# Optimization experiments

Measured on AMD Instinct MI355X. Metric: run time of the kernel, lower is better.

The kernel has to match this reference:

```python
import jax, jax.numpy as jnp
import numpy as np

N_NODES = 50000
N_EDGES = 1_600_000
IN_DIM = 64
HID_DIM = 64
OUT_DIM = 64


def setup_inputs() -> dict:
    key = jax.random.key(0)
    k = jax.random.split(key, 7)
    feat = jax.random.normal(k[0], (N_NODES, IN_DIM), dtype=jnp.float32)
    src = jax.random.randint(k[1], (N_EDGES,), 0, N_NODES, dtype=jnp.int32)
    dst = jax.random.randint(k[2], (N_EDGES,), 0, N_NODES, dtype=jnp.int32)
    # nn.init.normal_(weight, std=0.1); bias default uniform ~ small, use 0.1*randn
    W1 = 0.1 * jax.random.normal(k[3], (HID_DIM, IN_DIM), dtype=jnp.float32)
    b1 = 0.1 * jax.random.normal(k[4], (HID_DIM,), dtype=jnp.float32)
    W2 = 0.1 * jax.random.normal(k[5], (OUT_DIM, HID_DIM), dtype=jnp.float32)
    b2 = 0.1 * jax.random.normal(k[6], (OUT_DIM,), dtype=jnp.float32)
    return {"feat": feat, "src": src, "dst": dst, "W1": W1, "b1": b1, "W2": W2, "b2": b2}


def _gnn_layer(h, src, dst, W, b):
    # copy_u + sum: gather source-node features along edges, scatter-sum to dst
    agg = jax.ops.segment_sum(h[src], dst, num_segments=N_NODES)  # [N, d_in]
    return agg @ W.T + b  # nn.Linear


def reference(feat, src, dst, W1, b1, W2, b2):
    h = _gnn_layer(feat, src, dst, W1, b1)
    h = jnp.tanh(h)
    h = _gnn_layer(h, src, dst, W2, b2)
    return h
```

## Files before the change

kernel.cpp:

```cpp
#include <hip/hip_runtime.h>

#define N_NODES 50000
#define N_EDGES 1600000
#define DIM 64
#define NBK 196
#define BIN_BLOCKS 391
#define CSR_CAP 12288
#define QCAP 3072
#define GEMM_BLOCKS 197

__device__ __forceinline__ unsigned short f2bf(float f) {
    union { float f; unsigned u; } v; v.f = f;
    unsigned r = v.u + 0x7FFF + ((v.u >> 16) & 1);
    return (unsigned short)(r >> 16);
}
__device__ __forceinline__ float bf_lo(unsigned u) {
    union { unsigned u; float f; } v; v.u = u << 16;  return v.f;
}
__device__ __forceinline__ float bf_hi(unsigned u) {
    union { unsigned u; float f; } v; v.u = u & 0xFFFF0000u;  return v.f;
}
__device__ __forceinline__ float bf2f(unsigned short h) {
    union { unsigned u; float f; } v; v.u = ((unsigned)h) << 16;  return v.f;
}

__global__ __launch_bounds__(256) void bin_and_gemm1(const int* __restrict__ src,
                                                     const int* __restrict__ dst,
                                                     int* __restrict__ bcur,
                                                     int* __restrict__ binned,
                                                     const float* __restrict__ X,
                                                     const float* __restrict__ W,
                                                     unsigned short* __restrict__ T) {
    __shared__ int cnt[NBK];
    __shared__ int lofs[NBK];
    __shared__ int shiftv[NBK];
    __shared__ int sb[256];
    __shared__ int stag[4096];
    __shared__ unsigned char stb[4096];
    __shared__ float Ws[64 * 64];
    int tid = threadIdx.x;

    if (blockIdx.x >= BIN_BLOCKS) {
#pragma unroll
        for (int j = 0; j < 16; ++j) Ws[j * 256 + tid] = W[j * 256 + tid];
        __syncthreads();

        int n = (blockIdx.x - BIN_BLOCKS) * 256 + tid;
        if (n > N_NODES) return;
        ushort4* tp = (ushort4*)(T + (size_t)n * 64);
        if (n == N_NODES) {
            ushort4 z = {0, 0, 0, 0};
#pragma unroll
            for (int k = 0; k < 16; ++k) tp[k] = z;
            return;
        }

        float4 x[16];
        const float4* xp = (const float4*)(X + (size_t)n * 64);
#pragma unroll
        for (int k = 0; k < 16; ++k) x[k] = xp[k];

        for (int fg = 0; fg < 16; ++fg) {
            float r[4];
#pragma unroll
            for (int fi = 0; fi < 4; ++fi) {
                int f = fg * 4 + fi;
                float acc = 0.f;
#pragma unroll
                for (int k4 = 0; k4 < 16; ++k4) {
                    float4 w = *(const float4*)&Ws[f * 64 + k4 * 4];
                    float4 xv = x[k4];
                    acc += xv.x * w.x + xv.y * w.y + xv.z * w.z + xv.w * w.w;
                }
                r[fi] = acc;
            }
            ushort4 o;
            o.x = f2bf(r[0]); o.y = f2bf(r[1]); o.z = f2bf(r[2]); o.w = f2bf(r[3]);
            tp[fg] = o;
        }
        return;
    }

    if (tid < NBK) cnt[tid] = 0;
    __syncthreads();

    int base = blockIdx.x * 4096;
    int nedge = N_EDGES - base;
    if (nedge > 4096) nedge = 4096;

    int myb[16], myr[16], myp[16];
#pragma unroll
    for (int i = 0; i < 16; ++i) {
        int e = base + i * 256 + tid;
        myb[i] = -1;
        if (e < N_EDGES) {
            int s = src[e], d = dst[e];
            int b = d >> 8;
            myb[i] = b;
            myp[i] = ((d & 255) << 16) | s;
            myr[i] = atomicAdd(&cnt[b], 1);
        }
    }
    __syncthreads();

    int c = (tid < NBK) ? cnt[tid] : 0;
    sb[tid] = c;
    __syncthreads();
    for (int off = 1; off < 256; off <<= 1) {
        int u = (tid >= off) ? sb[tid - off] : 0;
        __syncthreads();
        sb[tid] += u;
        __syncthreads();
    }
    if (tid < NBK) {
        lofs[tid] = sb[tid] - c;
        if (c) shiftv[tid] = tid * CSR_CAP + atomicAdd(&bcur[tid * 16], c) - lofs[tid];
    }
    __syncthreads();

#pragma unroll
    for (int i = 0; i < 16; ++i) {
        if (myb[i] >= 0) {
            int idx = lofs[myb[i]] + myr[i];
            stag[idx] = myp[i];
            stb[idx] = (unsigned char)myb[i];
        }
    }
    __syncthreads();

    for (int i = tid; i < nedge; i += 256)
        binned[i + shiftv[stb[i]]] = stag[i];
}

__global__ __launch_bounds__(256) void build_csr(const int* __restrict__ binned,
                                                 const int* __restrict__ bcur,
                                                 unsigned* __restrict__ nodeinfo,
                                                 unsigned short* __restrict__ csr16) {
    __shared__ int cnt[64], cnt2[64], ofs[64], sb[64];
    __shared__ int qtot;
    int tid = threadIdx.x;
    int b = blockIdx.x >> 2;
    int q = blockIdx.x & 3;
    int ibase = b * CSR_CAP;
    int qbase = (b * 4 + q) * QCAP;
    int m = bcur[b * 16];
    if (m > CSR_CAP) m = CSR_CAP;
    if (tid < 64) { cnt[tid] = 0; cnt2[tid] = 0; }
    __syncthreads();

    for (int i = tid; i < m; i += 256) {
        int dl = (binned[ibase + i] >> 16) & 255;
        if ((dl >> 6) == q) atomicAdd(&cnt[dl & 63], 1);
    }
    __syncthreads();

    int v = 0;
    if (tid < 64) { v = (cnt[tid] + 15) & ~15; sb[tid] = v; }
    __syncthreads();
    for (int off = 1; off < 64; off <<= 1) {
        int u = (tid >= off && tid < 64) ? sb[tid - off] : 0;
        __syncthreads();
        if (tid < 64) sb[tid] += u;
        __syncthreads();
    }
    if (tid < 64) {
        ofs[tid] = sb[tid] - v;
        int node = (b << 8) + (q << 6) + tid;
        if (node < N_NODES)
            nodeinfo[node] = ((unsigned)v << 23) | (unsigned)(qbase + ofs[tid]);
    }
    if (tid == 63) qtot = sb[63];
    __syncthreads();

    int qt = qtot;
    for (int i = tid; i < qt; i += 256) csr16[qbase + i] = (unsigned short)N_NODES;
    __syncthreads();

    for (int i = tid; i < m; i += 256) {
        int p = binned[ibase + i];
        int dl = (p >> 16) & 255;
        if ((dl >> 6) == q) {
            int r = atomicAdd(&cnt2[dl & 63], 1);
            csr16[qbase + ofs[dl & 63] + r] = (unsigned short)(p & 0xFFFF);
        }
    }
}

__global__ __launch_bounds__(256) void gemm64_bf16(const unsigned short* __restrict__ X,
                                                   const float* __restrict__ W,
                                                   unsigned short* __restrict__ T,
                                                   int n_rows) {
    __shared__ float Ws[64 * 64];
    int tid = threadIdx.x;
#pragma unroll
    for (int j = 0; j < 16; ++j) Ws[j * 256 + tid] = W[j * 256 + tid];
    __syncthreads();

    int n = blockIdx.x * 256 + tid;
    if (n >= n_rows) {
        if (n == n_rows) {
            ushort4 z = {0, 0, 0, 0};
            ushort4* tp = (ushort4*)(T + (size_t)n * 64);
#pragma unroll
            for (int k = 0; k < 16; ++k) tp[k] = z;
        }
        return;
    }

    uint4 xr[8];
    const uint4* xp = (const uint4*)(X + (size_t)n * 64);
#pragma unroll
    for (int k = 0; k < 8; ++k) xr[k] = xp[k];
    float x[64];
    const unsigned* xu = (const unsigned*)xr;
#pragma unroll
    for (int p = 0; p < 32; ++p) {
        unsigned u = xu[p];
        x[2 * p] = bf_lo(u);
        x[2 * p + 1] = bf_hi(u);
    }

    const float4* xv4 = (const float4*)x;
    ushort4* tp = (ushort4*)(T + (size_t)n * 64);
    for (int fg = 0; fg < 16; ++fg) {
        float r[4];
#pragma unroll
        for (int fi = 0; fi < 4; ++fi) {
            int f = fg * 4 + fi;
            float acc = 0.f;
#pragma unroll
            for (int k4 = 0; k4 < 16; ++k4) {
                float4 w = *(const float4*)&Ws[f * 64 + k4 * 4];
                float4 xv = xv4[k4];
                acc += xv.x * w.x + xv.y * w.y + xv.z * w.z + xv.w * w.w;
            }
            r[fi] = acc;
        }
        ushort4 o;
        o.x = f2bf(r[0]); o.y = f2bf(r[1]); o.z = f2bf(r[2]); o.w = f2bf(r[3]);
        tp[fg] = o;
    }
}

__global__ __launch_bounds__(256) void aggregate(const unsigned short* __restrict__ T,
                                                 const unsigned short* __restrict__ csr,
                                                 const unsigned* __restrict__ nodeinfo,
                                                 const float* __restrict__ bias,
                                                 void* __restrict__ outp,
                                                 int mode) {
    int node = blockIdx.x * 4 + (threadIdx.x >> 6);
    int lane = threadIdx.x & 63;
    if (node >= N_NODES) return;
    unsigned info = nodeinfo[node];
    int pos = (int)(info & 0x7FFFFFu);
    int groups = (int)(info >> 23) >> 3;
    const uint4* ix = (const uint4*)(csr + pos);
    float acc = bias[lane];
    float acc2 = 0.f;
    for (int g = 0; g < groups; g += 2) {
        uint4 ia = ix[g];
        uint4 ib = ix[g + 1];
        int s0 = ia.x & 0xFFFF, s1 = ia.x >> 16;
        int s2 = ia.y & 0xFFFF, s3 = ia.y >> 16;
        int s4 = ia.z & 0xFFFF, s5 = ia.z >> 16;
        int s6 = ia.w & 0xFFFF, s7 = ia.w >> 16;
        int u0 = ib.x & 0xFFFF, u1 = ib.x >> 16;
        int u2 = ib.y & 0xFFFF, u3 = ib.y >> 16;
        int u4 = ib.z & 0xFFFF, u5 = ib.z >> 16;
        int u6 = ib.w & 0xFFFF, u7 = ib.w >> 16;
        unsigned short v0 = T[(size_t)s0 * DIM + lane];
        unsigned short v1 = T[(size_t)s1 * DIM + lane];
        unsigned short v2 = T[(size_t)s2 * DIM + lane];
        unsigned short v3 = T[(size_t)s3 * DIM + lane];
        unsigned short v4 = T[(size_t)s4 * DIM + lane];
        unsigned short v5 = T[(size_t)s5 * DIM + lane];
        unsigned short v6 = T[(size_t)s6 * DIM + lane];
        unsigned short v7 = T[(size_t)s7 * DIM + lane];
        unsigned short w0 = T[(size_t)u0 * DIM + lane];
        unsigned short w1 = T[(size_t)u1 * DIM + lane];
        unsigned short w2 = T[(size_t)u2 * DIM + lane];
        unsigned short w3 = T[(size_t)u3 * DIM + lane];
        unsigned short w4 = T[(size_t)u4 * DIM + lane];
        unsigned short w5 = T[(size_t)u5 * DIM + lane];
        unsigned short w6 = T[(size_t)u6 * DIM + lane];
        unsigned short w7 = T[(size_t)u7 * DIM + lane];
        acc  += (bf2f(v0) + bf2f(v1)) + (bf2f(v2) + bf2f(v3)) +
                (bf2f(v4) + bf2f(v5)) + (bf2f(v6) + bf2f(v7));
        acc2 += (bf2f(w0) + bf2f(w1)) + (bf2f(w2) + bf2f(w3)) +
                (bf2f(w4) + bf2f(w5)) + (bf2f(w6) + bf2f(w7));
    }
    acc += acc2;
    if (mode) {
        float e = __expf(2.f * acc);
        acc = 1.f - 2.f / (e + 1.f);
        ((unsigned short*)outp)[(size_t)node * DIM + lane] = f2bf(acc);
    } else {
        ((float*)outp)[(size_t)node * DIM + lane] = acc;
    }
}

extern "C" void kernel_launch(void* const* d_in, const int* in_sizes, int n_in,
                              void* d_out, int out_size, void* d_ws, size_t ws_size,
                              hipStream_t stream) {
    const float* feat = (const float*)d_in[0];
    const int*   src  = (const int*)d_in[1];
    const int*   dst  = (const int*)d_in[2];
    const float* W1   = (const float*)d_in[3];
    const float* b1   = (const float*)d_in[4];
    const float* W2   = (const float*)d_in[5];
    const float* b2   = (const float*)d_in[6];

    int*            binned   = (int*)d_ws;
    unsigned short* csr16    = (unsigned short*)(binned + NBK * CSR_CAP);
    unsigned*       nodeinfo = (unsigned*)(csr16 + NBK * 4 * QCAP);
    int*            bcur     = (int*)(nodeinfo + N_NODES);
    unsigned short* t        = (unsigned short*)(bcur + NBK * 16 + 8);

    unsigned short* h = (unsigned short*)d_out;
    float* out = (float*)d_out;

    const int NB = (N_NODES + 3) / 4;

    hipMemsetAsync(bcur, 0, NBK * 16 * sizeof(int), stream);
    bin_and_gemm1<<<BIN_BLOCKS + GEMM_BLOCKS, 256, 0, stream>>>(
        src, dst, bcur, binned, feat, W1, t);
    build_csr<<<NBK * 4, 256, 0, stream>>>(binned, bcur, nodeinfo, csr16);

    aggregate<<<NB, 256, 0, stream>>>(t, csr16, nodeinfo, b1, h, 1);

    gemm64_bf16<<<GEMM_BLOCKS, 256, 0, stream>>>(h, W2, t, N_NODES);
    aggregate<<<NB, 256, 0, stream>>>(t, csr16, nodeinfo, b2, out, 0);
}
```

Measured before the change: 243.9 us.

## Split feature table into two half-planes and gather 16-byte rows per lane in aggregate

The transformed feature table is stored as two 32-column bf16 planes instead of one 64-column array. The aggregate kernel launches twice as many blocks, one per half. Each wavefront handles 16 edges per iteration, with each lane loading 16 bytes (8 features) of one neighbour row, followed by a cross-lane shuffle reduction. This swaps many 2-byte scalar gathers for fewer wide vector loads, and each half-plane is a smaller working set that should fit better in cache. The cost is extra shuffle reduction work, index-selection logic, and twice as many index reads across blocks.

```diff
diff --git a/kernel.cpp b/kernel.cpp
--- a/kernel.cpp
+++ b/kernel.cpp
@@ -8,6 +8,8 @@
 #define CSR_CAP 12288
 #define QCAP 3072
 #define GEMM_BLOCKS 197
+#define NB_AGG 12500
+#define PLANE ((size_t)(N_NODES + 1) * 32)
 
 __device__ __forceinline__ unsigned short f2bf(float f) {
     union { float f; unsigned u; } v; v.f = f;
@@ -19,9 +21,6 @@
 }
 __device__ __forceinline__ float bf_hi(unsigned u) {
     union { unsigned u; float f; } v; v.u = u & 0xFFFF0000u;  return v.f;
-}
-__device__ __forceinline__ float bf2f(unsigned short h) {
-    union { unsigned u; float f; } v; v.u = ((unsigned)h) << 16;  return v.f;
 }
 
 __global__ __launch_bounds__(256) void bin_and_gemm1(const int* __restrict__ src,
@@ -30,7 +29,8 @@
                                                      int* __restrict__ binned,
                                                      const float* __restrict__ X,
                                                      const float* __restrict__ W,
-                                                     unsigned short* __restrict__ T) {
+                                                     unsigned short* __restrict__ T0,
+                                                     unsigned short* __restrict__ T1) {
     __shared__ int cnt[NBK];
     __shared__ int lofs[NBK];
     __shared__ int shiftv[NBK];
@@ -47,11 +47,12 @@
 
         int n = (blockIdx.x - BIN_BLOCKS) * 256 + tid;
         if (n > N_NODES) return;
-        ushort4* tp = (ushort4*)(T + (size_t)n * 64);
+        ushort4* t0 = (ushort4*)(T0 + (size_t)n * 32);
+        ushort4* t1 = (ushort4*)(T1 + (size_t)n * 32);
         if (n == N_NODES) {
             ushort4 z = {0, 0, 0, 0};
 #pragma unroll
-            for (int k = 0; k < 16; ++k) tp[k] = z;
+            for (int k = 0; k < 8; ++k) { t0[k] = z; t1[k] = z; }
             return;
         }
 
@@ -76,7 +77,7 @@
             }
             ushort4 o;
             o.x = f2bf(r[0]); o.y = f2bf(r[1]); o.z = f2bf(r[2]); o.w = f2bf(r[3]);
-            tp[fg] = o;
+            if (fg < 8) t0[fg] = o; else t1[fg - 8] = o;
         }
         return;
     }
@@ -188,7 +189,8 @@
 
 __global__ __launch_bounds__(256) void gemm64_bf16(const unsigned short* __restrict__ X,
                                                    const float* __restrict__ W,
-                                                   unsigned short* __restrict__ T,
+                                                   unsigned short* __restrict__ T0,
+                                                   unsigned short* __restrict__ T1,
                                                    int n_rows) {
     __shared__ float Ws[64 * 64];
     int tid = threadIdx.x;
@@ -197,13 +199,13 @@
     __syncthreads();
 
     int n = blockIdx.x * 256 + tid;
-    if (n >= n_rows) {
-        if (n == n_rows) {
-            ushort4 z = {0, 0, 0, 0};
-            ushort4* tp = (ushort4*)(T + (size_t)n * 64);
-#pragma unroll
-            for (int k = 0; k < 16; ++k) tp[k] = z;
-        }
+    if (n > n_rows) return;
+    ushort4* t0 = (ushort4*)(T0 + (size_t)n * 32);
+    ushort4* t1 = (ushort4*)(T1 + (size_t)n * 32);
+    if (n == n_rows) {
+        ushort4 z = {0, 0, 0, 0};
+#pragma unroll
+        for (int k = 0; k < 8; ++k) { t0[k] = z; t1[k] = z; }
         return;
     }
 
@@ -221,7 +223,6 @@
     }
 
     const float4* xv4 = (const float4*)x;
-    ushort4* tp = (ushort4*)(T + (size_t)n * 64);
     for (int fg = 0; fg < 16; ++fg) {
         float r[4];
 #pragma unroll
@@ -238,64 +239,77 @@
         }
         ushort4 o;
         o.x = f2bf(r[0]); o.y = f2bf(r[1]); o.z = f2bf(r[2]); o.w = f2bf(r[3]);
-        tp[fg] = o;
-    }
-}
-
-__global__ __launch_bounds__(256) void aggregate(const unsigned short* __restrict__ T,
+        if (fg < 8) t0[fg] = o; else t1[fg - 8] = o;
+    }
+}
+
+__global__ __launch_bounds__(256) void aggregate(const unsigned short* __restrict__ T0,
+                                                 const unsigned short* __restrict__ T1,
                                                  const unsigned short* __restrict__ csr,
                                                  const unsigned* __restrict__ nodeinfo,
                                                  const float* __restrict__ bias,
                                                  void* __restrict__ outp,
                                                  int mode) {
-    int node = blockIdx.x * 4 + (threadIdx.x >> 6);
+    int bidx = blockIdx.x;
+    int half = 0;
+    if (bidx >= NB_AGG) { half = 1; bidx -= NB_AGG; }
+    int node = bidx * 4 + (threadIdx.x >> 6);
     int lane = threadIdx.x & 63;
-    if (node >= N_NODES) return;
     unsigned info = nodeinfo[node];
     int pos = (int)(info & 0x7FFFFFu);
-    int groups = (int)(info >> 23) >> 3;
+    int iters = (int)(info >> 23) >> 4;
+    int j = lane >> 2;
+    int s4 = lane & 3;
+    int c = (j >> 1) & 3;
     const uint4* ix = (const uint4*)(csr + pos);
-    float acc = bias[lane];
-    float acc2 = 0.f;
-    for (int g = 0; g < groups; g += 2) {
-        uint4 ia = ix[g];
-        uint4 ib = ix[g + 1];
-        int s0 = ia.x & 0xFFFF, s1 = ia.x >> 16;
-        int s2 = ia.y & 0xFFFF, s3 = ia.y >> 16;
-        int s4 = ia.z & 0xFFFF, s5 = ia.z >> 16;
-        int s6 = ia.w & 0xFFFF, s7 = ia.w >> 16;
-        int u0 = ib.x & 0xFFFF, u1 = ib.x >> 16;
-        int u2 = ib.y & 0xFFFF, u3 = ib.y >> 16;
-        int u4 = ib.z & 0xFFFF, u5 = ib.z >> 16;
-        int u6 = ib.w & 0xFFFF, u7 = ib.w >> 16;
-        unsigned short v0 = T[(size_t)s0 * DIM + lane];
-        unsigned short v1 = T[(size_t)s1 * DIM + lane];
-        unsigned short v2 = T[(size_t)s2 * DIM + lane];
-        unsigned short v3 = T[(size_t)s3 * DIM + lane];
-        unsigned short v4 = T[(size_t)s4 * DIM + lane];
-        unsigned short v5 = T[(size_t)s5 * DIM + lane];
-        unsigned short v6 = T[(size_t)s6 * DIM + lane];
-        unsigned short v7 = T[(size_t)s7 * DIM + lane];
-        unsigned short w0 = T[(size_t)u0 * DIM + lane];
-        unsigned short w1 = T[(size_t)u1 * DIM + lane];
-        unsigned short w2 = T[(size_t)u2 * DIM + lane];
-        unsigned short w3 = T[(size_t)u3 * DIM + lane];
-        unsigned short w4 = T[(size_t)u4 * DIM + lane];
-        unsigned short w5 = T[(size_t)u5 * DIM + lane];
-        unsigned short w6 = T[(size_t)u6 * DIM + lane];
-        unsigned short w7 = T[(size_t)u7 * DIM + lane];
-        acc  += (bf2f(v0) + bf2f(v1)) + (bf2f(v2) + bf2f(v3)) +
-                (bf2f(v4) + bf2f(v5)) + (bf2f(v6) + bf2f(v7));
-        acc2 += (bf2f(w0) + bf2f(w1)) + (bf2f(w2) + bf2f(w3)) +
-                (bf2f(w4) + bf2f(w5)) + (bf2f(w6) + bf2f(w7));
-    }
-    acc += acc2;
-    if (mode) {
-        float e = __expf(2.f * acc);
-        acc = 1.f - 2.f / (e + 1.f);
-        ((unsigned short*)outp)[(size_t)node * DIM + lane] = f2bf(acc);
-    } else {
-        ((float*)outp)[(size_t)node * DIM + lane] = acc;
+    const char* Tb = (const char*)(half ? T1 : T0);
+    int fb = s4 * 16;
+
+    float a0 = 0.f, a1 = 0.f, a2 = 0.f, a3 = 0.f,
+          a4 = 0.f, a5 = 0.f, a6 = 0.f, a7 = 0.f;
+    for (int g = 0; g < iters; ++g) {
+        uint4 ia = ix[2 * g];
+        uint4 ib = ix[2 * g + 1];
+        uint4 sel = (j & 8) ? ib : ia;
+        unsigned w = (c == 0) ? sel.x : (c == 1) ? sel.y : (c == 2) ? sel.z : sel.w;
+        unsigned s = (j & 1) ? (w >> 16) : (w & 0xFFFFu);
+        uint4 r = *(const uint4*)(Tb + (size_t)s * 64 + fb);
+        a0 += bf_lo(r.x); a1 += bf_hi(r.x);
+        a2 += bf_lo(r.y); a3 += bf_hi(r.y);
+        a4 += bf_lo(r.z); a5 += bf_hi(r.z);
+        a6 += bf_lo(r.w); a7 += bf_hi(r.w);
+    }
+#pragma unroll
+    for (int mask = 4; mask <= 32; mask <<= 1) {
+        a0 += __shfl_xor(a0, mask, 64);
+        a1 += __shfl_xor(a1, mask, 64);
+        a2 += __shfl_xor(a2, mask, 64);
+        a3 += __shfl_xor(a3, mask, 64);
+        a4 += __shfl_xor(a4, mask, 64);
+        a5 += __shfl_xor(a5, mask, 64);
+        a6 += __shfl_xor(a6, mask, 64);
+        a7 += __shfl_xor(a7, mask, 64);
+    }
+    if (lane < 4) {
+        int col0 = half * 32 + lane * 8;
+        float av[8] = {a0, a1, a2, a3, a4, a5, a6, a7};
+#pragma unroll
+        for (int k = 0; k < 8; ++k) av[k] += bias[col0 + k];
+        if (mode) {
+            unsigned short hb[8];
+#pragma unroll
+            for (int k = 0; k < 8; ++k) {
+                float e = __expf(2.f * av[k]);
+                hb[k] = f2bf(1.f - 2.f / (e + 1.f));
+            }
+            ushort4* hp = (ushort4*)&((unsigned short*)outp)[(size_t)node * DIM + col0];
+            hp[0] = make_ushort4(hb[0], hb[1], hb[2], hb[3]);
+            hp[1] = make_ushort4(hb[4], hb[5], hb[6], hb[7]);
+        } else {
+            float4* op = (float4*)&((float*)outp)[(size_t)node * DIM + col0];
+            op[0] = make_float4(av[0], av[1], av[2], av[3]);
+            op[1] = make_float4(av[4], av[5], av[6], av[7]);
+        }
     }
 }
 
@@ -314,20 +328,19 @@
     unsigned short* csr16    = (unsigned short*)(binned + NBK * CSR_CAP);
     unsigned*       nodeinfo = (unsigned*)(csr16 + NBK * 4 * QCAP);
     int*            bcur     = (int*)(nodeinfo + N_NODES);
-    unsigned short* t        = (unsigned short*)(bcur + NBK * 16 + 8);
+    unsigned short* T0       = (unsigned short*)(bcur + NBK * 16 + 8);
+    unsigned short* T1       = T0 + PLANE;
 
     unsigned short* h = (unsigned short*)d_out;
     float* out = (float*)d_out;
 
-    const int NB = (N_NODES + 3) / 4;
-
     hipMemsetAsync(bcur, 0, NBK * 16 * sizeof(int), stream);
     bin_and_gemm1<<<BIN_BLOCKS + GEMM_BLOCKS, 256, 0, stream>>>(
-        src, dst, bcur, binned, feat, W1, t);
+        src, dst, bcur, binned, feat, W1, T0, T1);
     build_csr<<<NBK * 4, 256, 0, stream>>>(binned, bcur, nodeinfo, csr16);
 
-    aggregate<<<NB, 256, 0, stream>>>(t, csr16, nodeinfo, b1, h, 1);
-
-    gemm64_bf16<<<GEMM_BLOCKS, 256, 0, stream>>>(h, W2, t, N_NODES);
-    aggregate<<<NB, 256, 0, stream>>>(t, csr16, nodeinfo, b2, out, 0);
-}
+    aggregate<<<2 * NB_AGG, 256, 0, stream>>>(T0, T1, csr16, nodeinfo, b1, h, 1);
+
+    gemm64_bf16<<<GEMM_BLOCKS, 256, 0, stream>>>(h, W2, T0, T1, N_NODES);
+    aggregate<<<2 * NB_AGG, 256, 0, stream>>>(T0, T1, csr16, nodeinfo, b2, out, 0);
+}
```

New measurement: 313.7 us. +28.6%, slower.

## Count per-node degrees in binning pass and shrink shared memory and registers

Applied to the files above, without the earlier changes.

The binning kernel now keeps per-destination degree counts with global atomics, so build_csr no longer rescans the binned edges to count them. Padding fill becomes per-node. The two branches of the fused binning/GEMM kernel now share one union shared-memory buffer under a launch-bounds occupancy hint. Both GEMMs keep inputs packed as bf16 to cut register use, which also rounds layer-1 features to bf16 before the matmul. The cost is 1.6M extra global atomics on a 50k-entry array, plus a larger memset.

```diff
diff --git a/kernel.cpp b/kernel.cpp
--- a/kernel.cpp
+++ b/kernel.cpp
@@ -8,6 +8,7 @@
 #define CSR_CAP 12288
 #define QCAP 3072
 #define GEMM_BLOCKS 197
+#define NB_AGG 12500
 
 __device__ __forceinline__ unsigned short f2bf(float f) {
     union { float f; unsigned u; } v; v.f = f;
@@ -24,23 +25,19 @@
     union { unsigned u; float f; } v; v.u = ((unsigned)h) << 16;  return v.f;
 }
 
-__global__ __launch_bounds__(256) void bin_and_gemm1(const int* __restrict__ src,
-                                                     const int* __restrict__ dst,
-                                                     int* __restrict__ bcur,
-                                                     int* __restrict__ binned,
-                                                     const float* __restrict__ X,
-                                                     const float* __restrict__ W,
-                                                     unsigned short* __restrict__ T) {
-    __shared__ int cnt[NBK];
-    __shared__ int lofs[NBK];
-    __shared__ int shiftv[NBK];
-    __shared__ int sb[256];
-    __shared__ int stag[4096];
-    __shared__ unsigned char stb[4096];
-    __shared__ float Ws[64 * 64];
+__global__ __launch_bounds__(256, 4) void bin_and_gemm1(const int* __restrict__ src,
+                                                        const int* __restrict__ dst,
+                                                        int* __restrict__ bcur,
+                                                        int* __restrict__ ncnt,
+                                                        int* __restrict__ binned,
+                                                        const float* __restrict__ X,
+                                                        const float* __restrict__ W,
+                                                        unsigned short* __restrict__ T) {
+    __shared__ __align__(16) char smem[27008];
     int tid = threadIdx.x;
 
     if (blockIdx.x >= BIN_BLOCKS) {
+        float* Ws = (float*)smem;
 #pragma unroll
         for (int j = 0; j < 16; ++j) Ws[j * 256 + tid] = W[j * 256 + tid];
         __syncthreads();
@@ -55,10 +52,14 @@
             return;
         }
 
-        float4 x[16];
+        unsigned xq[32];
         const float4* xp = (const float4*)(X + (size_t)n * 64);
 #pragma unroll
-        for (int k = 0; k < 16; ++k) x[k] = xp[k];
+        for (int k = 0; k < 16; ++k) {
+            float4 xv = xp[k];
+            xq[2 * k]     = ((unsigned)f2bf(xv.y) << 16) | f2bf(xv.x);
+            xq[2 * k + 1] = ((unsigned)f2bf(xv.w) << 16) | f2bf(xv.z);
+        }
 
         for (int fg = 0; fg < 16; ++fg) {
             float r[4];
@@ -69,8 +70,9 @@
 #pragma unroll
                 for (int k4 = 0; k4 < 16; ++k4) {
                     float4 w = *(const float4*)&Ws[f * 64 + k4 * 4];
-                    float4 xv = x[k4];
-                    acc += xv.x * w.x + xv.y * w.y + xv.z * w.z + xv.w * w.w;
+                    unsigned p0 = xq[2 * k4], p1 = xq[2 * k4 + 1];
+                    acc += bf_lo(p0) * w.x + bf_hi(p0) * w.y +
+                           bf_lo(p1) * w.z + bf_hi(p1) * w.w;
                 }
                 r[fi] = acc;
             }
@@ -80,6 +82,13 @@
         }
         return;
     }
+
+    int* cnt    = (int*)smem;
+    int* lofs   = cnt + NBK;
+    int* shiftv = lofs + NBK;
+    int* sb     = shiftv + NBK;
+    int* stag   = sb + 256;
+    unsigned char* stb = (unsigned char*)(stag + 4096);
 
     if (tid < NBK) cnt[tid] = 0;
     __syncthreads();
@@ -99,6 +108,7 @@
             myb[i] = b;
             myp[i] = ((d & 255) << 16) | s;
             myr[i] = atomicAdd(&cnt[b], 1);
+            atomicAdd(&ncnt[d], 1);
         }
     }
     __syncthreads();
@@ -134,10 +144,10 @@
 
 __global__ __launch_bounds__(256) void build_csr(const int* __restrict__ binned,
                                                  const int* __restrict__ bcur,
+                                                 const int* __restrict__ ncnt,
                                                  unsigned* __restrict__ nodeinfo,
                                                  unsigned short* __restrict__ csr16) {
     __shared__ int cnt[64], cnt2[64], ofs[64], sb[64];
-    __shared__ int qtot;
     int tid = threadIdx.x;
     int b = blockIdx.x >> 2;
     int q = blockIdx.x & 3;
@@ -145,17 +155,16 @@
     int qbase = (b * 4 + q) * QCAP;
     int m = bcur[b * 16];
     if (m > CSR_CAP) m = CSR_CAP;
-    if (tid < 64) { cnt[tid] = 0; cnt2[tid] = 0; }
-    __syncthreads();
-
-    for (int i = tid; i < m; i += 256) {
-        int dl = (binned[ibase + i] >> 16) & 255;
-        if ((dl >> 6) == q) atomicAdd(&cnt[dl & 63], 1);
-    }
-    __syncthreads();
-
-    int v = 0;
-    if (tid < 64) { v = (cnt[tid] + 15) & ~15; sb[tid] = v; }
+    int node = (b << 8) + (q << 6) + tid;
+
+    int v = 0, c0 = 0;
+    if (tid < 64) {
+        c0 = (node < N_NODES) ? ncnt[node] : 0;
+        cnt[tid] = c0;
+        cnt2[tid] = 0;
+        v = (c0 + 15) & ~15;
+        sb[tid] = v;
+    }
     __syncthreads();
     for (int off = 1; off < 64; off <<= 1) {
         int u = (tid >= off && tid < 64) ? sb[tid - off] : 0;
@@ -165,15 +174,11 @@
     }
     if (tid < 64) {
         ofs[tid] = sb[tid] - v;
-        int node = (b << 8) + (q << 6) + tid;
         if (node < N_NODES)
             nodeinfo[node] = ((unsigned)v << 23) | (unsigned)(qbase + ofs[tid]);
-    }
-    if (tid == 63) qtot = sb[63];
-    __syncthreads();
-
-    int qt = qtot;
-    for (int i = tid; i < qt; i += 256) csr16[qbase + i] = (unsigned short)N_NODES;
+        int o = qbase + ofs[tid];
+        for (int i = c0; i < v; ++i) csr16[o + i] = (unsigned short)N_NODES;
+    }
     __syncthreads();
 
     for (int i = tid; i < m; i += 256) {
@@ -211,16 +216,8 @@
     const uint4* xp = (const uint4*)(X + (size_t)n * 64);
 #pragma unroll
     for (int k = 0; k < 8; ++k) xr[k] = xp[k];
-    float x[64];
-    const unsigned* xu = (const unsigned*)xr;
-#pragma unroll
-    for (int p = 0; p < 32; ++p) {
-        unsigned u = xu[p];
-        x[2 * p] = bf_lo(u);
-        x[2 * p + 1] = bf_hi(u);
-    }
-
-    const float4* xv4 = (const float4*)x;
+    const unsigned* xq = (const unsigned*)xr;
+
     ushort4* tp = (ushort4*)(T + (size_t)n * 64);
     for (int fg = 0; fg < 16; ++fg) {
         float r[4];
@@ -231,8 +228,9 @@
 #pragma unroll
             for (int k4 = 0; k4 < 16; ++k4) {
                 float4 w = *(const float4*)&Ws[f * 64 + k4 * 4];
-                float4 xv = xv4[k4];
-                acc += xv.x * w.x + xv.y * w.y + xv.z * w.z + xv.w * w.w;
+                unsigned p0 = xq[2 * k4], p1 = xq[2 * k4 + 1];
+                acc += bf_lo(p0) * w.x + bf_hi(p0) * w.y +
+                       bf_lo(p1) * w.z + bf_hi(p1) * w.w;
             }
             r[fi] = acc;
         }
@@ -314,20 +312,19 @@
     unsigned short* csr16    = (unsigned short*)(binned + NBK * CSR_CAP);
     unsigned*       nodeinfo = (unsigned*)(csr16 + NBK * 4 * QCAP);
     int*            bcur     = (int*)(nodeinfo + N_NODES);
-    unsigned short* t        = (unsigned short*)(bcur + NBK * 16 + 8);
+    int*            ncnt     = bcur + NBK * 16;
+    unsigned short* t        = (unsigned short*)(ncnt + N_NODES);
 
     unsigned short* h = (unsigned short*)d_out;
     float* out = (float*)d_out;
 
-    const int NB = (N_NODES + 3) / 4;
-
-    hipMemsetAsync(bcur, 0, NBK * 16 * sizeof(int), stream);
+    hipMemsetAsync(bcur, 0, (NBK * 16 + N_NODES) * sizeof(int), stream);
     bin_and_gemm1<<<BIN_BLOCKS + GEMM_BLOCKS, 256, 0, stream>>>(
-        src, dst, bcur, binned, feat, W1, t);
-    build_csr<<<NBK * 4, 256, 0, stream>>>(binned, bcur, nodeinfo, csr16);
-
-    aggregate<<<NB, 256, 0, stream>>>(t, csr16, nodeinfo, b1, h, 1);
+        src, dst, bcur, ncnt, binned, feat, W1, t);
+    build_csr<<<NBK * 4, 256, 0, stream>>>(binned, bcur, ncnt, nodeinfo, csr16);
+
+    aggregate<<<NB_AGG, 256, 0, stream>>>(t, csr16, nodeinfo, b1, h, 1);
 
     gemm64_bf16<<<GEMM_BLOCKS, 256, 0, stream>>>(h, W2, t, N_NODES);
-    aggregate<<<NB, 256, 0, stream>>>(t, csr16, nodeinfo, b2, out, 0);
-}
+    aggregate<<<NB_AGG, 256, 0, stream>>>(t, csr16, nodeinfo, b2, out, 0);
+}
```

After: 537.8 us. +120.5%, slower.

## Fuse layer-2 linear transform into first aggregation epilogue

Applied to the files above, without the earlier changes.

Removes the separate gemm64_bf16 kernel and the bf16 intermediate h buffer by having the first aggregation compute tanh into shared memory and immediately multiply by W2 (loaded transposed into LDS per block). Output goes to a separate workspace buffer t2, and the zero sentinel row is written by block 0. This saves one launch and one full round trip of node features through global memory, but each block now stages 16KB of W2 into LDS, which may reduce occupancy of the latency-bound gather kernel.

```diff
diff --git a/kernel.cpp b/kernel.cpp
--- a/kernel.cpp
+++ b/kernel.cpp
@@ -8,17 +8,12 @@
 #define CSR_CAP 12288
 #define QCAP 3072
 #define GEMM_BLOCKS 197
+#define NB_AGG 12500
 
 __device__ __forceinline__ unsigned short f2bf(float f) {
     union { float f; unsigned u; } v; v.f = f;
     unsigned r = v.u + 0x7FFF + ((v.u >> 16) & 1);
     return (unsigned short)(r >> 16);
-}
-__device__ __forceinline__ float bf_lo(unsigned u) {
-    union { unsigned u; float f; } v; v.u = u << 16;  return v.f;
-}
-__device__ __forceinline__ float bf_hi(unsigned u) {
-    union { unsigned u; float f; } v; v.u = u & 0xFFFF0000u;  return v.f;
 }
 __device__ __forceinline__ float bf2f(unsigned short h) {
     union { unsigned u; float f; } v; v.u = ((unsigned)h) << 16;  return v.f;
@@ -186,68 +181,87 @@
     }
 }
 
-__global__ __launch_bounds__(256) void gemm64_bf16(const unsigned short* __restrict__ X,
-                                                   const float* __restrict__ W,
-                                                   unsigned short* __restrict__ T,
-                                                   int n_rows) {
-    __shared__ float Ws[64 * 64];
-    int tid = threadIdx.x;
-#pragma unroll
-    for (int j = 0; j < 16; ++j) Ws[j * 256 + tid] = W[j * 256 + tid];
-    __syncthreads();
-
-    int n = blockIdx.x * 256 + tid;
-    if (n >= n_rows) {
-        if (n == n_rows) {
-            ushort4 z = {0, 0, 0, 0};
-            ushort4* tp = (ushort4*)(T + (size_t)n * 64);
-#pragma unroll
-            for (int k = 0; k < 16; ++k) tp[k] = z;
-        }
-        return;
-    }
-
-    uint4 xr[8];
-    const uint4* xp = (const uint4*)(X + (size_t)n * 64);
-#pragma unroll
-    for (int k = 0; k < 8; ++k) xr[k] = xp[k];
-    float x[64];
-    const unsigned* xu = (const unsigned*)xr;
-#pragma unroll
-    for (int p = 0; p < 32; ++p) {
-        unsigned u = xu[p];
-        x[2 * p] = bf_lo(u);
-        x[2 * p + 1] = bf_hi(u);
-    }
-
-    const float4* xv4 = (const float4*)x;
-    ushort4* tp = (ushort4*)(T + (size_t)n * 64);
-    for (int fg = 0; fg < 16; ++fg) {
-        float r[4];
-#pragma unroll
-        for (int fi = 0; fi < 4; ++fi) {
-            int f = fg * 4 + fi;
-            float acc = 0.f;
-#pragma unroll
-            for (int k4 = 0; k4 < 16; ++k4) {
-                float4 w = *(const float4*)&Ws[f * 64 + k4 * 4];
-                float4 xv = xv4[k4];
-                acc += xv.x * w.x + xv.y * w.y + xv.z * w.z + xv.w * w.w;
-            }
-            r[fi] = acc;
-        }
-        ushort4 o;
-        o.x = f2bf(r[0]); o.y = f2bf(r[1]); o.z = f2bf(r[2]); o.w = f2bf(r[3]);
-        tp[fg] = o;
-    }
-}
-
-__global__ __launch_bounds__(256) void aggregate(const unsigned short* __restrict__ T,
+__global__ __launch_bounds__(256) void agg_fuse1(const unsigned short* __restrict__ T,
                                                  const unsigned short* __restrict__ csr,
                                                  const unsigned* __restrict__ nodeinfo,
-                                                 const float* __restrict__ bias,
-                                                 void* __restrict__ outp,
-                                                 int mode) {
+                                                 const float* __restrict__ b1,
+                                                 const float* __restrict__ W2,
+                                                 unsigned short* __restrict__ T2) {
+    __shared__ float4 W2t4[1024];
+    __shared__ float hsf[4 * 64];
+    int tid = threadIdx.x;
+    int w = tid >> 6;
+    int lane = tid & 63;
+    int node = blockIdx.x * 4 + w;
+
+    for (int L4 = tid; L4 < 1024; L4 += 256) {
+        int k4 = L4 >> 6, f = L4 & 63;
+        W2t4[L4] = *(const float4*)(W2 + f * 64 + k4 * 4);
+    }
+
+    unsigned info = nodeinfo[node];
+    int pos = (int)(info & 0x7FFFFFu);
+    int groups = (int)(info >> 23) >> 3;
+    const uint4* ix = (const uint4*)(csr + pos);
+    float acc = b1[lane];
+    float acc2 = 0.f;
+    for (int g = 0; g < groups; g += 2) {
+        uint4 ia = ix[g];
+        uint4 ib = ix[g + 1];
+        int s0 = ia.x & 0xFFFF, s1 = ia.x >> 16;
+        int s2 = ia.y & 0xFFFF, s3 = ia.y >> 16;
+        int s4 = ia.z & 0xFFFF, s5 = ia.z >> 16;
+        int s6 = ia.w & 0xFFFF, s7 = ia.w >> 16;
+        int u0 = ib.x & 0xFFFF, u1 = ib.x >> 16;
+        int u2 = ib.y & 0xFFFF, u3 = ib.y >> 16;
+        int u4 = ib.z & 0xFFFF, u5 = ib.z >> 16;
+        int u6 = ib.w & 0xFFFF, u7 = ib.w >> 16;
+        unsigned short v0 = T[(size_t)s0 * DIM + lane];
+        unsigned short v1 = T[(size_t)s1 * DIM + lane];
+        unsigned short v2 = T[(size_t)s2 * DIM + lane];
+        unsigned short v3 = T[(size_t)s3 * DIM + lane];
+        unsigned short v4 = T[(size_t)s4 * DIM + lane];
+        unsigned short v5 = T[(size_t)s5 * DIM + lane];
+        unsigned short v6 = T[(size_t)s6 * DIM + lane];
+        unsigned short v7 = T[(size_t)s7 * DIM + lane];
+        unsigned short w0 = T[(size_t)u0 * DIM + lane];
+        unsigned short w1 = T[(size_t)u1 * DIM + lane];
+        unsigned short w2 = T[(size_t)u2 * DIM + lane];
+        unsigned short w3 = T[(size_t)u3 * DIM + lane];
+        unsigned short w4 = T[(size_t)u4 * DIM + lane];
+        unsigned short w5 = T[(size_t)u5 * DIM + lane];
+        unsigned short w6 = T[(size_t)u6 * DIM + lane];
+        unsigned short w7 = T[(size_t)u7 * DIM + lane];
+        acc  += (bf2f(v0) + bf2f(v1)) + (bf2f(v2) + bf2f(v3)) +
+                (bf2f(v4) + bf2f(v5)) + (bf2f(v6) + bf2f(v7));
+        acc2 += (bf2f(w0) + bf2f(w1)) + (bf2f(w2) + bf2f(w3)) +
+                (bf2f(w4) + bf2f(w5)) + (bf2f(w6) + bf2f(w7));
+    }
+    acc += acc2;
+
+    float e = __expf(2.f * acc);
+    hsf[w * 64 + lane] = 1.f - 2.f / (e + 1.f);
+    __syncthreads();
+
+    const float4* hv4 = (const float4*)&hsf[w * 64];
+    float tf = 0.f;
+#pragma unroll
+    for (int k4 = 0; k4 < 16; ++k4) {
+        float4 hv = hv4[k4];
+        float4 wv = W2t4[k4 * 64 + lane];
+        tf += hv.x * wv.x + hv.y * wv.y + hv.z * wv.z + hv.w * wv.w;
+    }
+    T2[(size_t)node * DIM + lane] = f2bf(tf);
+
+    if (blockIdx.x == 0 && tid < 64)
+        T2[(size_t)N_NODES * DIM + tid] = 0;
+}
+
+__global__ __launch_bounds__(256) void agg_out(const unsigned short* __restrict__ T,
+                                               const unsigned short* __restrict__ csr,
+                                               const unsigned* __restrict__ nodeinfo,
+                                               const float* __restrict__ bias,
+                                               float* __restrict__ outp) {
     int node = blockIdx.x * 4 + (threadIdx.x >> 6);
     int lane = threadIdx.x & 63;
     if (node >= N_NODES) return;
@@ -290,13 +304,7 @@
                 (bf2f(w4) + bf2f(w5)) + (bf2f(w6) + bf2f(w7));
     }
     acc += acc2;
-    if (mode) {
-        float e = __expf(2.f * acc);
-        acc = 1.f - 2.f / (e + 1.f);
-        ((unsigned short*)outp)[(size_t)node * DIM + lane] = f2bf(acc);
-    } else {
-        ((float*)outp)[(size_t)node * DIM + lane] = acc;
-    }
+    outp[(size_t)node * DIM + lane] = acc;
 }
 
 extern "C" void kernel_launch(void* const* d_in, const int* in_sizes, int n_in,
@@ -309,25 +317,21 @@
     const float* b1   = (const float*)d_in[4];
     const float* W2   = (const float*)d_in[5];
     const float* b2   = (const float*)d_in[6];
+    float* out = (float*)d_out;
 
     int*            binned   = (int*)d_ws;
     unsigned short* csr16    = (unsigned short*)(binned + NBK * CSR_CAP);
     unsigned*       nodeinfo = (unsigned*)(csr16 + NBK * 4 * QCAP);
     int*            bcur     = (int*)(nodeinfo + N_NODES);
     unsigned short* t        = (unsigned short*)(bcur + NBK * 16 + 8);
-
-    unsigned short* h = (unsigned short*)d_out;
-    float* out = (float*)d_out;
-
-    const int NB = (N_NODES + 3) / 4;
+    unsigned short* t2       = t + (size_t)(N_NODES + 1) * 64;
 
     hipMemsetAsync(bcur, 0, NBK * 16 * sizeof(int), stream);
     bin_and_gemm1<<<BIN_BLOCKS + GEMM_BLOCKS, 256, 0, stream>>>(
         src, dst, bcur, binned, feat, W1, t);
     build_csr<<<NBK * 4, 256, 0, stream>>>(binned, bcur, nodeinfo, csr16);
 
-    aggregate<<<NB, 256, 0, stream>>>(t, csr16, nodeinfo, b1, h, 1);
-
-    gemm64_bf16<<<GEMM_BLOCKS, 256, 0, stream>>>(h, W2, t, N_NODES);
-    aggregate<<<NB, 256, 0, stream>>>(t, csr16, nodeinfo, b2, out, 0);
-}
+    agg_fuse1<<<NB_AGG, 256, 0, stream>>>(t, csr16, nodeinfo, b1, W2, t2);
+
+    agg_out<<<NB_AGG, 256, 0, stream>>>(t2, csr16, nodeinfo, b2, out);
+}
```

Result: faster. 232.7 us (-4.6%).
